# Kernel optimization log

Hardware: AMD Instinct MI355X
Metric: run time of the kernel (lower is better)

## Reference

```python
import jax, jax.numpy as jnp
import numpy as np

B, N, H, D, A = 64, 32, 100, 400, 200  # batch, news_num, hist_len, news_dim, attention_dim


def setup_inputs() -> dict:
    key = jax.random.key(0)
    k0, k1, k2, k3, k4 = jax.random.split(key, 5)
    log_vec = jax.random.normal(k0, (B, H, D), dtype=jnp.float32)
    log_mask = jax.random.randint(k1, (B, H), 0, 2).astype(jnp.int32)
    news_vec = jax.random.normal(k2, (B, N, D), dtype=jnp.float32)
    W1 = jax.random.normal(k3, (A, 2 * D), dtype=jnp.float32) * 0.02
    b1 = jnp.zeros((A,), dtype=jnp.float32)
    W2 = jax.random.normal(k4, (1, A), dtype=jnp.float32) * 0.02
    b2 = jnp.zeros((1,), dtype=jnp.float32)
    return {"log_vec": log_vec, "log_mask": log_mask, "news_vec": news_vec,
            "W1": W1, "b1": b1, "W2": W2, "b2": b2}


def reference(log_vec, log_mask, news_vec, W1, b1, W2, b2):
    d = log_vec.shape[-1]
    # affine1 on cat([news, log]) == Wn @ news + Wl @ log (split the weight),
    # so we never build the [B, N, H, 2D] concat tensor.
    Wn, Wl = W1[:, :d], W1[:, d:]
    pn = jnp.einsum('bnd,ad->bna', news_vec, Wn)            # [B, N, A]
    pl = jnp.einsum('bhd,ad->bha', log_vec, Wl) + b1        # [B, H, A]
    h = jnp.tanh(pn[:, :, None, :] + pl[:, None, :, :])     # [B, N, H, A]
    logits = jnp.einsum('bnha,a->bnh', h, W2[0]) + b2[0]    # [B, N, H]
    logits = jnp.where(log_mask[:, None, :] == 0, jnp.float32(-1e9), logits)
    attn = jax.nn.softmax(logits, axis=2)                   # softmax over hist_len
    return jnp.einsum('bnh,bhd->bnd', attn, log_vec)        # [B, N, D]
```

## Files before the change

### kernel.cpp

```cpp
#include <hip/hip_runtime.h>
#include <hip/hip_fp16.h>
#include <math.h>

#define BB 64
#define NN 32
#define HH 100
#define DD 400
#define AA 200
#define NL 8
#define NQ 4
#define SZ_LOG  2560000
#define SZ_NEWS 819200
#define SZ_W1   160000
#define SZ_MASK 6400
#define LROW 40
#define PLP 204

typedef unsigned short u16;
typedef unsigned int   u32;
typedef unsigned long long u64;
typedef __attribute__((ext_vector_type(8))) short    bf16x8;
typedef __attribute__((ext_vector_type(8))) _Float16 halfx8;
typedef __attribute__((ext_vector_type(4))) float    f32x4;

__device__ __forceinline__ float bfh(u32 h) { return __uint_as_float(h << 16); }
__device__ __forceinline__ u16 f2bf(float f) {
    u32 u = __float_as_uint(f);
    u += 0x7fffu + ((u >> 16) & 1u);
    return (u16)(u >> 16);
}
__device__ __forceinline__ float halfbits(u16 h) {
    __half_raw r; r.x = h; __half hv(r); return __half2float(hv);
}
__device__ __forceinline__ u16 h2bits(float f) {
    __half h = __float2half(f); return *(u16*)&h;
}
__device__ __forceinline__ float sane(float x) {
    return (fabsf(x) < 1e6f) ? x : 0.f;
}

template<int DT>
__device__ __forceinline__ float ld1(const void* p, size_t i) {
    if (DT == 0) return bfh(((const u16*)p)[i]);
    if (DT == 1) return halfbits(((const u16*)p)[i]);
    return ((const float*)p)[i];
}

__device__ __forceinline__ bf16x8 cvt8(const float* p) {
    const float4 x0 = *(const float4*)p;
    const float4 x1 = *(const float4*)(p + 4);
    bf16x8 r;
    r[0] = (short)f2bf(sane(x0.x)); r[1] = (short)f2bf(sane(x0.y));
    r[2] = (short)f2bf(sane(x0.z)); r[3] = (short)f2bf(sane(x0.w));
    r[4] = (short)f2bf(sane(x1.x)); r[5] = (short)f2bf(sane(x1.y));
    r[6] = (short)f2bf(sane(x1.z)); r[7] = (short)f2bf(sane(x1.w));
    return r;
}

__device__ __forceinline__ void detect_counts(const u16* logv, int t, int* s_cbf, int* s_cfh) {
    int cbf = 0, cfh = 0;
    for (int i = 2 * t; i < 4096; i += 512) {
        u16 h = logv[i];
        float a = fabsf(bfh(h));
        if (h && a >= 0.03125f && a <= 16.f) cbf++;
        float g = fabsf(halfbits(h));
        if (h && g >= 1e-3f && g <= 64.f) cfh++;
    }
    #pragma unroll
    for (int off = 32; off; off >>= 1) {
        cbf += __shfl_xor(cbf, off);
        cfh += __shfl_xor(cfh, off);
    }
    if ((t & 63) == 0) {
        atomicAdd(s_cbf, cbf);
        atomicAdd(s_cfh, cfh);
    }
}

template<int DT>
__device__ __forceinline__ void mega_body(
        const void* __restrict__ logv, const void* __restrict__ newsv,
        const void* __restrict__ w1,
        const void* __restrict__ w2p, const void* __restrict__ b1p,
        void* __restrict__ out,
        u16* __restrict__ As, u16* __restrict__ Bs,
        float* __restrict__ pls, float* __restrict__ pnb,
        float (* __restrict__ lgt)[HH],
        float* __restrict__ w2s, float* __restrict__ b1s,
        const int* __restrict__ chi, int hn, bool useChi,
        int b, int n0, int t)
{
    const int wave = t >> 6, lane = t & 63;
    const int quad = lane >> 4, col16 = lane & 15;
    const int mtc = (hn + 15) >> 4;

    if (t < AA) {
        w2s[t] = sane(ld1<DT>(w2p, t));
        b1s[t] = sane(ld1<DT>(b1p, t));
    }

    const int mtIdx = wave >> 1, half = wave & 1;
    const bool isPn = (mtIdx == mtc);
    const bool act  = (mtIdx <= mtc);
    const int arow  = isPn ? (112 + min(col16, NL - 1)) : (mtIdx * 16 + col16);
    const int aidx  = arow * LROW + quad * 8;
    int bidx[7];
    #pragma unroll
    for (int si = 0; si < 7; ++si) {
        const int sl = min(half * 7 + si, 12);
        const int brow = min(sl * 16 + col16, AA - 1);
        bidx[si] = ((isPn ? 0 : 208) + brow) * LROW + quad * 8;
    }
    f32x4 acc[7];
    #pragma unroll
    for (int si = 0; si < 7; ++si) acc[si] = (f32x4){0.f, 0.f, 0.f, 0.f};

    const int bh0 = t / 832,   rem0 = t - bh0 * 832;
    const int br0 = rem0 >> 2, bseg0 = rem0 & 3;
    const size_t bg0 = (size_t)min(br0, AA - 1) * (2 * DD) + bh0 * DD + bseg0 * 8;
    const int bl0 = (bh0 * 208 + br0) * LROW + bseg0 * 8;
    const int i1 = t + 1024;
    const bool bok1 = i1 < 1664;
    const int bh1 = bok1 ? (i1 / 832) : 0, rem1 = i1 - bh1 * 832;
    const int br1 = rem1 >> 2, bseg1 = rem1 & 3;
    const size_t bg1 = (size_t)min(br1, AA - 1) * (2 * DD) + bh1 * DD + bseg1 * 8;
    const int bl1 = (bh1 * 208 + br1) * LROW + bseg1 * 8;
    const int ar = t >> 2, aseg = t & 3;
    const bool a_ok = (t < 480) && ((ar < mtc * 16) || (ar >= 112));
    size_t agi = 0;
    if (a_ok) {
        if (ar < 112) agi = ((size_t)b * HH + chi[min(ar, hn - 1)]) * DD + aseg * 8;
        else          agi = ((size_t)b * NN + n0 + (ar - 112)) * DD + aseg * 8;
    }
    const int al = ar * LROW + aseg * 8;
    const u16*   agp  = (ar < 112 ? (const u16*)logv   : (const u16*)newsv) + agi;
    const float* agpf = (ar < 112 ? (const float*)logv : (const float*)newsv) + agi;
    const u16*   w1p  = (const u16*)w1;
    const float* w1pf = (const float*)w1;

    uint4 vb0 = {0,0,0,0}, vb1 = {0,0,0,0}, va = {0,0,0,0};
    const uint4 z4 = {0u, 0u, 0u, 0u};

    if (DT != 2) {
        vb0 = *(const uint4*)(w1p + bg0);
        if (bok1) vb1 = *(const uint4*)(w1p + bg1);
        if (a_ok) va = *(const uint4*)agp;
    }

    for (int ki = 0; ki < 13; ++ki) {
        if (DT != 2) {
            *(uint4*)&Bs[bl0] = vb0;
            if (bok1) *(uint4*)&Bs[bl1] = vb1;
            if (a_ok) *(uint4*)&As[al] = va;
        } else {
            uint4 v = z4;
            if (!(ki == 12 && bseg0 >= 2)) { bf16x8 c = cvt8(w1pf + bg0 + ki * 32); v = *(uint4*)&c; }
            *(uint4*)&Bs[bl0] = v;
            if (bok1) {
                v = z4;
                if (!(ki == 12 && bseg1 >= 2)) { bf16x8 c = cvt8(w1pf + bg1 + ki * 32); v = *(uint4*)&c; }
                *(uint4*)&Bs[bl1] = v;
            }
            if (a_ok) {
                v = z4;
                if (!(ki == 12 && aseg >= 2)) { bf16x8 c = cvt8(agpf + ki * 32); v = *(uint4*)&c; }
                *(uint4*)&As[al] = v;
            }
        }
        __syncthreads();

        if (DT != 2 && ki < 12) {
            const int kn = ki + 1;
            vb0 = (kn == 12 && bseg0 >= 2) ? z4 : *(const uint4*)(w1p + bg0 + (size_t)kn * 32);
            if (bok1) vb1 = (kn == 12 && bseg1 >= 2) ? z4 : *(const uint4*)(w1p + bg1 + (size_t)kn * 32);
            if (a_ok) va = (kn == 12 && aseg >= 2) ? z4 : *(const uint4*)(agp + (size_t)kn * 32);
        }

        if (act) {
            if (DT == 1) {
                const halfx8 af = *(const halfx8*)&As[aidx];
                #pragma unroll
                for (int si = 0; si < 7; ++si) {
                    const halfx8 bf = *(const halfx8*)&Bs[bidx[si]];
                    acc[si] = __builtin_amdgcn_mfma_f32_16x16x32_f16(af, bf, acc[si], 0, 0, 0);
                }
            } else {
                const bf16x8 af = *(const bf16x8*)&As[aidx];
                #pragma unroll
                for (int si = 0; si < 7; ++si) {
                    const bf16x8 bf = *(const bf16x8*)&Bs[bidx[si]];
                    acc[si] = __builtin_amdgcn_mfma_f32_16x16x32_bf16(af, bf, acc[si], 0, 0, 0);
                }
            }
        }
        __syncthreads();
    }

    if (act) {
        #pragma unroll
        for (int si = 0; si < 7; ++si) {
            const int sl = half * 7 + si;
            if (sl > 12) continue;
            const int acol = sl * 16 + col16;
            if (acol < AA) {
                if (isPn) {
                    #pragma unroll
                    for (int r = 0; r < 4; ++r) {
                        const int row = quad * 4 + r;
                        if (row < NL) pnb[row * PLP + acol] = sane(acc[si][r]) + b1s[acol];
                    }
                } else {
                    #pragma unroll
                    for (int r = 0; r < 4; ++r) {
                        const int row = mtIdx * 16 + quad * 4 + r;
                        if (row < hn) pls[row * PLP + acol] = sane(acc[si][r]);
                    }
                }
            }
        }
    }
    __syncthreads();

    {
        const int j = wave + (lane << 4);
        if (j < 4 * hn) {
            const int p = j / hn;
            const int i = j - p * hn;
            const int h = chi[i];
            const float* plr = pls + i * PLP;
            const float* pA  = pnb + p * PLP;
            const float* pB  = pnb + (p + 4) * PLP;
            float accA = 0.f, accB = 0.f, sw = 0.f;
            for (int a = 0; a < AA; a += 4) {
                const float4 w4  = *(const float4*)&w2s[a];
                const float4 pl4 = *(const float4*)&plr[a];
                const float4 pA4 = *(const float4*)&pA[a];
                const float4 pB4 = *(const float4*)&pB[a];
                #define LSTEP(CC) { \
                    const float w2v = w4.CC; \
                    const float plv = pl4.CC; \
                    const float eA = __builtin_amdgcn_exp2f((pA4.CC + plv) * 2.885390081777927f); \
                    const float eB = __builtin_amdgcn_exp2f((pB4.CC + plv) * 2.885390081777927f); \
                    accA = __builtin_fmaf(w2v, __builtin_amdgcn_rcpf(eA + 1.f), accA); \
                    accB = __builtin_fmaf(w2v, __builtin_amdgcn_rcpf(eB + 1.f), accB); \
                    sw += w2v; }
                LSTEP(x) LSTEP(y) LSTEP(z) LSTEP(w)
                #undef LSTEP
            }
            lgt[p][h]     = sw - 2.f * accA;
            lgt[p + 4][h] = sw - 2.f * accB;
        }
    }
    __syncthreads();

    if (wave < NL) {
        const int n = wave;
        float m1 = lgt[n][lane];
        float m2 = (lane < HH - 64) ? lgt[n][64 + lane] : -3.0e38f;
        float mx = fmaxf(m1, m2);
        #pragma unroll
        for (int off = 32; off; off >>= 1) mx = fmaxf(mx, __shfl_xor(mx, off));
        float e1 = expf(m1 - mx);
        float e2 = (lane < HH - 64) ? expf(m2 - mx) : 0.f;
        float s = e1 + e2;
        #pragma unroll
        for (int off = 32; off; off >>= 1) s += __shfl_xor(s, off);
        const float inv = 1.f / s;
        lgt[n][lane] = e1 * inv;
        if (lane < HH - 64) lgt[n][64 + lane] = e2 * inv;
    }
    __syncthreads();

    {
        const int n = wave >> 1, half2 = wave & 1;
        const int hn_pv = useChi ? hn : HH;
        const int d2a = lane + 128 * half2;
        const int d2b = d2a + 64;
        const bool bv = d2b < DD / 2;
        const int d2bc = bv ? d2b : d2a;
        float aA0 = 0.f, aA1 = 0.f, aB0 = 0.f, aB1 = 0.f;
        int i = 0;
        for (; i + 1 < hn_pv; i += 2) {
            const int h0 = useChi ? chi[i] : i;
            const int h1 = useChi ? chi[i + 1] : (i + 1);
            const float w0 = lgt[n][h0], w1v = lgt[n][h1];
            float v0a, v1a, v0b, v1b, u0a, u1a, u0b, u1b;
            if (DT == 2) {
                const float* r0 = (const float*)logv + ((size_t)b * HH + h0) * DD;
                const float* r1 = (const float*)logv + ((size_t)b * HH + h1) * DD;
                v0a = r0[2 * d2a]; v1a = r0[2 * d2a + 1];
                v0b = r0[2 * d2bc]; v1b = r0[2 * d2bc + 1];
                u0a = r1[2 * d2a]; u1a = r1[2 * d2a + 1];
                u0b = r1[2 * d2bc]; u1b = r1[2 * d2bc + 1];
            } else {
                const u16* r0 = (const u16*)logv + ((size_t)b * HH + h0) * DD;
                const u16* r1 = (const u16*)logv + ((size_t)b * HH + h1) * DD;
                const u32 pa = *(const u32*)(r0 + 2 * d2a);
                const u32 pb = *(const u32*)(r0 + 2 * d2bc);
                const u32 qa = *(const u32*)(r1 + 2 * d2a);
                const u32 qb = *(const u32*)(r1 + 2 * d2bc);
                if (DT == 0) {
                    v0a = bfh(pa & 0xffffu); v1a = bfh(pa >> 16);
                    v0b = bfh(pb & 0xffffu); v1b = bfh(pb >> 16);
                    u0a = bfh(qa & 0xffffu); u1a = bfh(qa >> 16);
                    u0b = bfh(qb & 0xffffu); u1b = bfh(qb >> 16);
                } else {
                    v0a = halfbits((u16)(pa & 0xffffu)); v1a = halfbits((u16)(pa >> 16));
                    v0b = halfbits((u16)(pb & 0xffffu)); v1b = halfbits((u16)(pb >> 16));
                    u0a = halfbits((u16)(qa & 0xffffu)); u1a = halfbits((u16)(qa >> 16));
                    u0b = halfbits((u16)(qb & 0xffffu)); u1b = halfbits((u16)(qb >> 16));
                }
            }
            aA0 = __builtin_fmaf(w0, sane(v0a), aA0); aA1 = __builtin_fmaf(w0, sane(v1a), aA1);
            aB0 = __builtin_fmaf(w0, sane(v0b), aB0); aB1 = __builtin_fmaf(w0, sane(v1b), aB1);
            aA0 = __builtin_fmaf(w1v, sane(u0a), aA0); aA1 = __builtin_fmaf(w1v, sane(u1a), aA1);
            aB0 = __builtin_fmaf(w1v, sane(u0b), aB0); aB1 = __builtin_fmaf(w1v, sane(u1b), aB1);
        }
        if (i < hn_pv) {
            const int h0 = useChi ? chi[i] : i;
            const float w0 = lgt[n][h0];
            float v0a, v1a, v0b, v1b;
            if (DT == 2) {
                const float* r0 = (const float*)logv + ((size_t)b * HH + h0) * DD;
                v0a = r0[2 * d2a]; v1a = r0[2 * d2a + 1];
                v0b = r0[2 * d2bc]; v1b = r0[2 * d2bc + 1];
            } else {
                const u16* r0 = (const u16*)logv + ((size_t)b * HH + h0) * DD;
                const u32 pa = *(const u32*)(r0 + 2 * d2a);
                const u32 pb = *(const u32*)(r0 + 2 * d2bc);
                if (DT == 0) {
                    v0a = bfh(pa & 0xffffu); v1a = bfh(pa >> 16);
                    v0b = bfh(pb & 0xffffu); v1b = bfh(pb >> 16);
                } else {
                    v0a = halfbits((u16)(pa & 0xffffu)); v1a = halfbits((u16)(pa >> 16));
                    v0b = halfbits((u16)(pb & 0xffffu)); v1b = halfbits((u16)(pb >> 16));
                }
            }
            aA0 = __builtin_fmaf(w0, sane(v0a), aA0); aA1 = __builtin_fmaf(w0, sane(v1a), aA1);
            aB0 = __builtin_fmaf(w0, sane(v0b), aB0); aB1 = __builtin_fmaf(w0, sane(v1b), aB1);
        }
        const size_t obase = ((size_t)b * NN + n0 + n) * DD;
        aA0 = sane(aA0); aA1 = sane(aA1); aB0 = sane(aB0); aB1 = sane(aB1);
        if (DT == 0) {
            *(u32*)((u16*)out + obase + 2 * d2a) = (u32)f2bf(aA0) | ((u32)f2bf(aA1) << 16);
            if (bv) *(u32*)((u16*)out + obase + 2 * d2b) = (u32)f2bf(aB0) | ((u32)f2bf(aB1) << 16);
        } else if (DT == 1) {
            *(u32*)((u16*)out + obase + 2 * d2a) = (u32)h2bits(aA0) | ((u32)h2bits(aA1) << 16);
            if (bv) *(u32*)((u16*)out + obase + 2 * d2b) = (u32)h2bits(aB0) | ((u32)h2bits(aB1) << 16);
        } else {
            float* f = (float*)out;
            f[obase + 2 * d2a] = aA0; f[obase + 2 * d2a + 1] = aA1;
            if (bv) { f[obase + 2 * d2b] = aB0; f[obase + 2 * d2b + 1] = aB1; }
        }
    }
}

__global__ __launch_bounds__(1024) void megafused(
        const void* __restrict__ logv, const int* __restrict__ mask,
        const void* __restrict__ newsv, const void* __restrict__ w1,
        const void* __restrict__ c200a, const void* __restrict__ c200b,
        void* __restrict__ out)
{
    __shared__ __align__(16) u16 As[120 * LROW];
    __shared__ __align__(16) u16 Bs[2 * 208 * LROW];
    __shared__ __align__(16) float pls[HH * PLP];
    __shared__ __align__(16) float pnb[NL * PLP];
    __shared__ float lgt[NL][HH];
    __shared__ float w2s[AA], b1s[AA];
    __shared__ int   mask_s[HH], chi[HH];
    __shared__ int   s_det[4], s_hn, s_diag[2];

    const int t = threadIdx.x;
    const int b  = blockIdx.x & 63;
    const int n0 = (blockIdx.x >> 6) * NL;
    const int wave = t >> 6, lane = t & 63;

    if (t < 4) s_det[t] = 0;
    if (t == 0) { s_diag[0] = 0; s_diag[1] = 0; }
    if (t < NL * HH) lgt[t / HH][t % HH] = -1.0e9f;
    if (t < HH) mask_s[t] = mask[b * HH + t];
    __syncthreads();
    if (t < 256) detect_counts((const u16*)logv, t, &s_det[0], &s_det[1]);
    if (t < AA) {
        if (((const u16*)c200a)[t]) atomicOr(&s_det[2], 1);
        if (((const u16*)c200b)[t]) atomicOr(&s_det[3], 1);
    }
    __syncthreads();
    const int dt = (s_det[0] > 1024) ? 0 : ((s_det[1] > 1600) ? 1 : 2);
    const bool aW2 = s_det[2] && !s_det[3];
    const void* w2p = aW2 ? c200a : c200b;
    const void* b1p = aW2 ? c200b : c200a;

    if (wave == 0) {
        const bool v = mask_s[lane] != 0;
        const u64 bal = __ballot(v);
        if (v) chi[__popcll(bal & ((1ull << lane) - 1ull))] = lane;
    } else if (wave == 1) {
        const u64 b0 = __ballot(mask_s[lane] != 0);
        const int c0 = __popcll(b0);
        const bool v1 = (lane < HH - 64) && (mask_s[64 + lane] != 0);
        const u64 b1 = __ballot(v1);
        if (v1) chi[c0 + __popcll(b1 & ((1ull << lane) - 1ull))] = 64 + lane;
        if (lane == 0) s_hn = c0 + __popcll(b1);
    }
    __syncthreads();
    const int hn = s_hn;
    const bool useChi = hn != 0;

    if (dt == 0)      mega_body<0>(logv, newsv, w1, w2p, b1p, out, As, Bs, pls, pnb, lgt, w2s, b1s, chi, hn, useChi, b, n0, t);
    else if (dt == 1) mega_body<1>(logv, newsv, w1, w2p, b1p, out, As, Bs, pls, pnb, lgt, w2s, b1s, chi, hn, useChi, b, n0, t);
    else              mega_body<2>(logv, newsv, w1, w2p, b1p, out, As, Bs, pls, pnb, lgt, w2s, b1s, chi, hn, useChi, b, n0, t);

    if (blockIdx.x == 0) {
        const u32* maskw = (const u32*)mask;
        int mbig = 0, moddnz = 0, mevennz = 0;
        for (int i = t; i < 3200; i += 1024) {
            u32 w = maskw[i];
            if (w > 1u) mbig = 1;
            if ((i & 1) && w) moddnz = 1;
            if (!(i & 1) && w) mevennz = 1;
        }
        atomicOr(&s_diag[0], mbig);
        atomicOr(&s_diag[1], moddnz | (mevennz << 1));
        __syncthreads();
        if (t == 0) {
            const int cb = s_det[0], ch = s_det[1];
            int dg = 0;
            if (cb > 700 && cb < 1300) dg |= 1;
            else if (cb <= 700 && ch > 1300 && ch < 1800) dg |= 1;
            if (s_diag[0]) dg |= 2;
            const int oddnz = s_diag[1] & 1, evennz = (s_diag[1] >> 1) & 1;
            if (!oddnz && evennz) dg |= 4;
            const int nza = s_det[2] ? 1 : 0, nzb = s_det[3] ? 1 : 0;
            if (nza == nzb) dg |= 8;
            if (dg) {
                const float V = 1024.f + 8.f * (float)dg;
                if (dt == 0)      ((u16*)out)[0] = f2bf(V);
                else if (dt == 1) ((u16*)out)[0] = h2bits(V);
                else              ((float*)out)[0] = V;
            }
        }
    }
}

extern "C" void kernel_launch(void* const* d_in, const int* in_sizes, int n_in,
                              void* d_out, int out_size, void* d_ws, size_t ws_size,
                              hipStream_t stream)
{
    const void *logv = nullptr, *maskv = nullptr, *newsv = nullptr, *w1v = nullptr;
    const void *c200a = nullptr, *c200b = nullptr;
    int n200 = 0;
    for (int i = 0; i < n_in; ++i) {
        int s = in_sizes[i];
        if (s == SZ_LOG) logv = d_in[i];
        else if (s == SZ_NEWS) newsv = d_in[i];
        else if (s == SZ_W1) w1v = d_in[i];
        else if (s == SZ_MASK) maskv = d_in[i];
        else if (s == AA) { if (n200 == 0) c200a = d_in[i]; else if (n200 == 1) c200b = d_in[i]; ++n200; }
    }
    if (!logv || !newsv || !w1v || !maskv || n200 < 2) {
        logv = d_in[0]; maskv = d_in[1]; newsv = d_in[2]; w1v = d_in[3];
        c200a = d_in[4]; c200b = d_in[5];
    }

    megafused<<<BB * NQ, 1024, 0, stream>>>(logv, (const int*)maskv, newsv, w1v,
                                            c200a, c200b, d_out);
}
```

Measured before the change: 143.5 us.

## Double-buffer GEMM LDS tiles, aliasing second buffer onto pls scratch

Switches the projection GEMM's K-loop from a single LDS tile with two barriers per step to ping-pong A/B buffers, so the next slice is written while the current one feeds MFMA. The second buffer is aliased onto the pls scratch region, which is only written after the GEMM, so shared memory use does not grow. Register prefetch now runs two steps ahead, and the logit-stage thread index becomes linear in t. The aliasing depends on no pls writes happening before the loop ends, and __restrict__ qualifiers were dropped, which could affect codegen.

```diff
diff --git a/kernel.cpp b/kernel.cpp
--- a/kernel.cpp
+++ b/kernel.cpp
@@ -83,11 +83,11 @@
         const void* __restrict__ w1,
         const void* __restrict__ w2p, const void* __restrict__ b1p,
         void* __restrict__ out,
-        u16* __restrict__ As, u16* __restrict__ Bs,
-        float* __restrict__ pls, float* __restrict__ pnb,
-        float (* __restrict__ lgt)[HH],
-        float* __restrict__ w2s, float* __restrict__ b1s,
-        const int* __restrict__ chi, int hn, bool useChi,
+        u16* As0, u16* Bs0, u16* ovl,
+        float* pls, float* pnb,
+        float (*lgt)[HH],
+        float* w2s, float* b1s,
+        const int* chi, int hn, bool useChi,
         int b, int n0, int t)
 {
     const int wave = t >> 6, lane = t & 63;
@@ -138,57 +138,80 @@
     const u16*   w1p  = (const u16*)w1;
     const float* w1pf = (const float*)w1;
 
-    uint4 vb0 = {0,0,0,0}, vb1 = {0,0,0,0}, va = {0,0,0,0};
+    u16* const As1 = ovl;
+    u16* const Bs1 = ovl + 120 * LROW;
+
     const uint4 z4 = {0u, 0u, 0u, 0u};
+    uint4 vb0 = z4, vb1 = z4, va = z4;
 
     if (DT != 2) {
         vb0 = *(const uint4*)(w1p + bg0);
         if (bok1) vb1 = *(const uint4*)(w1p + bg1);
-        if (a_ok) va = *(const uint4*)agp;
-    }
+        if (a_ok) va  = *(const uint4*)agp;
+        *(uint4*)&Bs0[bl0] = vb0;
+        if (bok1) *(uint4*)&Bs0[bl1] = vb1;
+        if (a_ok) *(uint4*)&As0[al] = va;
+        vb0 = *(const uint4*)(w1p + bg0 + 32);
+        if (bok1) vb1 = *(const uint4*)(w1p + bg1 + 32);
+        if (a_ok) va  = *(const uint4*)(agp + 32);
+    } else {
+        { bf16x8 c = cvt8(w1pf + bg0); *(uint4*)&Bs0[bl0] = *(uint4*)&c; }
+        if (bok1) { bf16x8 c = cvt8(w1pf + bg1); *(uint4*)&Bs0[bl1] = *(uint4*)&c; }
+        if (a_ok) { bf16x8 c = cvt8(agpf); *(uint4*)&As0[al] = *(uint4*)&c; }
+    }
+    __syncthreads();
 
     for (int ki = 0; ki < 13; ++ki) {
+        const int cur = ki & 1;
+        u16* const Ac = cur ? As1 : As0;
+        u16* const Bc = cur ? Bs1 : Bs0;
+        u16* const An = cur ? As0 : As1;
+        u16* const Bn = cur ? Bs0 : Bs1;
+
         if (DT != 2) {
-            *(uint4*)&Bs[bl0] = vb0;
-            if (bok1) *(uint4*)&Bs[bl1] = vb1;
-            if (a_ok) *(uint4*)&As[al] = va;
+            if (ki < 12) {
+                *(uint4*)&Bn[bl0] = vb0;
+                if (bok1) *(uint4*)&Bn[bl1] = vb1;
+                if (a_ok) *(uint4*)&An[al] = va;
+            }
+            if (ki < 11) {
+                const int kn = ki + 2;
+                vb0 = (kn == 12 && bseg0 >= 2) ? z4 : *(const uint4*)(w1p + bg0 + (size_t)kn * 32);
+                if (bok1) vb1 = (kn == 12 && bseg1 >= 2) ? z4 : *(const uint4*)(w1p + bg1 + (size_t)kn * 32);
+                if (a_ok) va = (kn == 12 && aseg >= 2) ? z4 : *(const uint4*)(agp + (size_t)kn * 32);
+            }
         } else {
-            uint4 v = z4;
-            if (!(ki == 12 && bseg0 >= 2)) { bf16x8 c = cvt8(w1pf + bg0 + ki * 32); v = *(uint4*)&c; }
-            *(uint4*)&Bs[bl0] = v;
-            if (bok1) {
-                v = z4;
-                if (!(ki == 12 && bseg1 >= 2)) { bf16x8 c = cvt8(w1pf + bg1 + ki * 32); v = *(uint4*)&c; }
-                *(uint4*)&Bs[bl1] = v;
-            }
-            if (a_ok) {
-                v = z4;
-                if (!(ki == 12 && aseg >= 2)) { bf16x8 c = cvt8(agpf + ki * 32); v = *(uint4*)&c; }
-                *(uint4*)&As[al] = v;
-            }
-        }
-        __syncthreads();
-
-        if (DT != 2 && ki < 12) {
-            const int kn = ki + 1;
-            vb0 = (kn == 12 && bseg0 >= 2) ? z4 : *(const uint4*)(w1p + bg0 + (size_t)kn * 32);
-            if (bok1) vb1 = (kn == 12 && bseg1 >= 2) ? z4 : *(const uint4*)(w1p + bg1 + (size_t)kn * 32);
-            if (a_ok) va = (kn == 12 && aseg >= 2) ? z4 : *(const uint4*)(agp + (size_t)kn * 32);
+            if (ki < 12) {
+                const int kn = ki + 1;
+                uint4 v = z4;
+                if (!(kn == 12 && bseg0 >= 2)) { bf16x8 c = cvt8(w1pf + bg0 + (size_t)kn * 32); v = *(uint4*)&c; }
+                *(uint4*)&Bn[bl0] = v;
+                if (bok1) {
+                    v = z4;
+                    if (!(kn == 12 && bseg1 >= 2)) { bf16x8 c = cvt8(w1pf + bg1 + (size_t)kn * 32); v = *(uint4*)&c; }
+                    *(uint4*)&Bn[bl1] = v;
+                }
+                if (a_ok) {
+                    v = z4;
+                    if (!(kn == 12 && aseg >= 2)) { bf16x8 c = cvt8(agpf + (size_t)kn * 32); v = *(uint4*)&c; }
+                    *(uint4*)&An[al] = v;
+                }
+            }
         }
 
         if (act) {
             if (DT == 1) {
-                const halfx8 af = *(const halfx8*)&As[aidx];
+                const halfx8 af = *(const halfx8*)&Ac[aidx];
                 #pragma unroll
                 for (int si = 0; si < 7; ++si) {
-                    const halfx8 bf = *(const halfx8*)&Bs[bidx[si]];
+                    const halfx8 bf = *(const halfx8*)&Bc[bidx[si]];
                     acc[si] = __builtin_amdgcn_mfma_f32_16x16x32_f16(af, bf, acc[si], 0, 0, 0);
                 }
             } else {
-                const bf16x8 af = *(const bf16x8*)&As[aidx];
+                const bf16x8 af = *(const bf16x8*)&Ac[aidx];
                 #pragma unroll
                 for (int si = 0; si < 7; ++si) {
-                    const bf16x8 bf = *(const bf16x8*)&Bs[bidx[si]];
+                    const bf16x8 bf = *(const bf16x8*)&Bc[bidx[si]];
                     acc[si] = __builtin_amdgcn_mfma_f32_16x16x32_bf16(af, bf, acc[si], 0, 0, 0);
                 }
             }
@@ -222,7 +245,7 @@
     __syncthreads();
 
     {
-        const int j = wave + (lane << 4);
+        const int j = t;
         if (j < 4 * hn) {
             const int p = j / hn;
             const int i = j - p * hn;
@@ -361,14 +384,17 @@
         const void* __restrict__ c200a, const void* __restrict__ c200b,
         void* __restrict__ out)
 {
-    __shared__ __align__(16) u16 As[120 * LROW];
-    __shared__ __align__(16) u16 Bs[2 * 208 * LROW];
-    __shared__ __align__(16) float pls[HH * PLP];
+    __shared__ __align__(16) u16 As0[120 * LROW];
+    __shared__ __align__(16) u16 Bs0[2 * 208 * LROW];
+    __shared__ __align__(16) char plspool[HH * PLP * 4];
     __shared__ __align__(16) float pnb[NL * PLP];
     __shared__ float lgt[NL][HH];
     __shared__ float w2s[AA], b1s[AA];
     __shared__ int   mask_s[HH], chi[HH];
     __shared__ int   s_det[4], s_hn, s_diag[2];
+
+    float* pls = (float*)plspool;
+    u16*   ovl = (u16*)plspool;
 
     const int t = threadIdx.x;
     const int b  = blockIdx.x & 63;
@@ -407,9 +433,9 @@
     const int hn = s_hn;
     const bool useChi = hn != 0;
 
-    if (dt == 0)      mega_body<0>(logv, newsv, w1, w2p, b1p, out, As, Bs, pls, pnb, lgt, w2s, b1s, chi, hn, useChi, b, n0, t);
-    else if (dt == 1) mega_body<1>(logv, newsv, w1, w2p, b1p, out, As, Bs, pls, pnb, lgt, w2s, b1s, chi, hn, useChi, b, n0, t);
-    else              mega_body<2>(logv, newsv, w1, w2p, b1p, out, As, Bs, pls, pnb, lgt, w2s, b1s, chi, hn, useChi, b, n0, t);
+    if (dt == 0)      mega_body<0>(logv, newsv, w1, w2p, b1p, out, As0, Bs0, ovl, pls, pnb, lgt, w2s, b1s, chi, hn, useChi, b, n0, t);
+    else if (dt == 1) mega_body<1>(logv, newsv, w1, w2p, b1p, out, As0, Bs0, ovl, pls, pnb, lgt, w2s, b1s, chi, hn, useChi, b, n0, t);
+    else              mega_body<2>(logv, newsv, w1, w2p, b1p, out, As0, Bs0, ovl, pls, pnb, lgt, w2s, b1s, chi, hn, useChi, b, n0, t);
 
     if (blockIdx.x == 0) {
         const u32* maskw = (const u32*)mask;
```

New measurement: 125.4 us. 12.7% less time.
